# Kernel optimization log

Hardware: AMD Instinct MI355X
Metric: run time of the kernel (lower is better)

Reference implementation:

```python
import jax, jax.numpy as jnp
import numpy as np

COST_CLASS, COST_OBJECTNESS, COST_GIOU, COST_CENTER = 1.0, 0.5, 2.0, 1.0
B, Q, G, C = 32, 4096, 32, 128


def setup_inputs() -> dict:
    key = jax.random.key(0)
    ks = jax.random.split(key, 6)
    return {
        "sem_cls_prob": jax.random.uniform(ks[0], (B, Q, C), jnp.float32),
        "objectness_prob": jax.random.uniform(ks[1], (B, Q), jnp.float32),
        "center_dist": jax.random.uniform(ks[2], (B, Q, G), jnp.float32),
        "gious": jax.random.uniform(ks[3], (B, Q, G), jnp.float32) * 2.0 - 1.0,  # gIoU in [-1,1]
        "gt_box_sem_cls_label": jax.random.randint(ks[4], (B, G), 0, C).astype(jnp.int64),
        "nactual_gt": jax.random.randint(ks[5], (B,), 1, G + 1).astype(jnp.int64),
    }


def _lsa(Cmat):
    """Jonker-Volgenant shortest augmenting path Hungarian.
    Cmat: [n, m] float64 with n <= m. Returns p: [m+1] int64, p[j] = row matched
    to column j (or -1), index m is the virtual start column. Equivalent to
    scipy.optimize.linear_sum_assignment on Cmat (modulo ties)."""
    n, m = Cmat.shape
    u = np.zeros(n, np.float64)
    v = np.zeros(m + 1, np.float64)
    p = np.full(m + 1, -1, np.int64)
    way = np.zeros(m, np.int64)
    for i in range(n):
        p[m] = i
        j0 = m
        minv = np.full(m, np.inf)
        used = np.zeros(m + 1, bool)
        while True:
            used[j0] = True
            i0 = p[j0]
            cur = Cmat[i0] - u[i0] - v[:m]            # vectorized Dijkstra relaxation
            better = (~used[:m]) & (cur < minv)
            minv = np.where(better, cur, minv)
            way = np.where(better, j0, way)
            mv = np.where(used[:m], np.inf, minv)
            j1 = int(np.argmin(mv))
            delta = mv[j1]
            rows = p[used]                            # matched rows of used cols (distinct)
            u[rows] += delta
            v[used] -= delta
            minv = np.where(used[:m], minv, minv - delta)
            j0 = j1
            if p[j0] == -1:
                break
        while j0 != m:                                # augment along the path
            j1 = way[j0]
            p[j0] = p[j1]
            j0 = j1
    return p


def hungarian_assign(final_cost, nactual_gt):
    """final_cost: np [B,Q,G]; emulates the per-batch scipy loop of the module."""
    Bn, Qn, _ = final_cost.shape
    per_prop = np.zeros((Bn, Qn), np.int64)
    mask = np.zeros((Bn, Qn), np.float32)
    for b in range(Bn):
        ng = int(nactual_gt[b])
        if ng > 0:
            p = _lsa(final_cost[b, :, :ng].T.astype(np.float64))  # [ng, Q]
            cols = np.nonzero(p[:Qn] >= 0)[0]
            per_prop[b, cols] = p[cols]
            mask[b, cols] = 1.0
    return per_prop, mask


def build_cost(sem_cls_prob, objectness_prob, center_dist, gious, gt_box_sem_cls_label):
    Bn, Qn, _ = sem_cls_prob.shape
    Gn = gt_box_sem_cls_label.shape[1]
    idx = jnp.broadcast_to(gt_box_sem_cls_label[:, None, :], (Bn, Qn, Gn))
    class_mat = -jnp.take_along_axis(sem_cls_prob, idx, axis=2)        # [B,Q,G]
    return (COST_CLASS * class_mat
            - COST_OBJECTNESS * objectness_prob[:, :, None]
            + COST_CENTER * center_dist
            - COST_GIOU * gious)


def reference(sem_cls_prob, objectness_prob, center_dist, gious, gt_box_sem_cls_label, nactual_gt):
    final_cost = build_cost(sem_cls_prob, objectness_prob, center_dist, gious, gt_box_sem_cls_label)
    cost_np = np.asarray(jax.device_get(final_cost))
    per_prop, mask = hungarian_assign(cost_np, np.asarray(jax.device_get(nactual_gt)))
    return jnp.asarray(per_prop), jnp.asarray(mask)
```

## Files before the change

kernel.cpp:

```cpp
#include <hip/hip_runtime.h>
#include <math.h>

#define NB   32
#define BQ   4096
#define GMAX 32
#define NC   128
#define BS   512
#define CPT  (BQ / BS)
#define NWAVE (BS / 64)

#define TQ   32
#define BBS  256

__launch_bounds__(BBS)
__global__ void build_cost_kernel(const float* __restrict__ sem,
                                  const float* __restrict__ objp,
                                  const float* __restrict__ cent,
                                  const float* __restrict__ giou,
                                  const int*   __restrict__ labels,
                                  const int*   __restrict__ nact,
                                  float* __restrict__ cost)
{
    const int b  = blockIdx.y;
    const int q0 = blockIdx.x * TQ;
    const int tid = threadIdx.x;

    __shared__ float sem_sh[TQ][NC + 1];
    __shared__ float cent_sh[TQ][GMAX + 1];
    __shared__ float giou_sh[TQ][GMAX + 1];
    __shared__ int lab_sh[GMAX];

    if (tid < GMAX) lab_sh[tid] = labels[b * GMAX + tid];
    const int ng = nact[b];

    const float4* semb = (const float4*)(sem + ((size_t)b * BQ + q0) * NC);
#pragma unroll
    for (int r = tid; r < TQ * NC / 4; r += BBS) {
        float4 vv = semb[r];
        int e = r * 4;
        int qq = e >> 7;
        int cc = e & (NC - 1);
        sem_sh[qq][cc]     = vv.x;
        sem_sh[qq][cc + 1] = vv.y;
        sem_sh[qq][cc + 2] = vv.z;
        sem_sh[qq][cc + 3] = vv.w;
    }
    {
        const float4* centb = (const float4*)(cent + ((size_t)b * BQ + q0) * GMAX);
        const float4* gioub = (const float4*)(giou + ((size_t)b * BQ + q0) * GMAX);
        int r = tid;
        float4 cv = centb[r];
        float4 gv = gioub[r];
        int e = r * 4;
        int qq = e >> 5;
        int ii = e & (GMAX - 1);
        cent_sh[qq][ii]     = cv.x;
        cent_sh[qq][ii + 1] = cv.y;
        cent_sh[qq][ii + 2] = cv.z;
        cent_sh[qq][ii + 3] = cv.w;
        giou_sh[qq][ii]     = gv.x;
        giou_sh[qq][ii + 1] = gv.y;
        giou_sh[qq][ii + 2] = gv.z;
        giou_sh[qq][ii + 3] = gv.w;
    }
    __syncthreads();

    const int qi = tid & (TQ - 1);
    const int ig = tid >> 5;
    const int q  = q0 + qi;
    const float ho = __fmul_rn(0.5f, objp[b * BQ + q]);

    for (int i = ig; i < ng; i += 8) {
        float pcls = sem_sh[qi][lab_sh[i]];
        float ce   = cent_sh[qi][i];
        float gi   = giou_sh[qi][i];
        float c = __fsub_rn(__fadd_rn(__fsub_rn(-pcls, ho), ce),
                            __fmul_rn(2.0f, gi));
        cost[((size_t)b * GMAX + i) * BQ + q] = c;
    }
}

__launch_bounds__(BS, 1)
__global__ void matcher_kernel(const float* __restrict__ cost,
                               const int*   __restrict__ nact,
                               float* __restrict__ out)
{
    const int b    = blockIdx.x;
    const int tid  = threadIdx.x;
    const int m    = BQ;
    const int wave = tid >> 6;
    const int lane = tid & 63;

    __shared__ __align__(16) short p_lds[BQ + 8];
    __shared__ __align__(16) unsigned short way_lds[BQ];
    __shared__ double u_lds[GMAX];
    __shared__ double   redv[2][NWAVE];
    __shared__ unsigned redpk[2][NWAVE];
    __shared__ int    step_i0[GMAX + 2];
    __shared__ double step_D[GMAX + 2];
    __shared__ float  rmin_v[GMAX];
    __shared__ int    rmin_j[GMAX];
    __shared__ int    unmatched[GMAX];
    __shared__ int    s_nunm;

    for (int k = tid; k < BQ + 8; k += BS) p_lds[k] = -1;
    const int ng = nact[b];
    const float* cb = cost + (size_t)b * GMAX * BQ;
    __syncthreads();

    for (int r = wave; r < ng; r += NWAVE) {
        const float4* row4 = (const float4*)(cb + (size_t)r * BQ);
        float bv = INFINITY; int bj = 0;
#pragma unroll
        for (int it = 0; it < 16; it++) {
            float4 vv = row4[lane + 64 * it];
            int j = (lane + 64 * it) * 4;
            if (vv.x < bv) { bv = vv.x; bj = j; }
            if (vv.y < bv) { bv = vv.y; bj = j + 1; }
            if (vv.z < bv) { bv = vv.z; bj = j + 2; }
            if (vv.w < bv) { bv = vv.w; bj = j + 3; }
        }
#pragma unroll
        for (int off = 32; off >= 1; off >>= 1) {
            float ov = __shfl_down(bv, off, 64);
            int   oj = __shfl_down(bj, off, 64);
            if (ov < bv || (ov == bv && oj < bj)) { bv = ov; bj = oj; }
        }
        if (lane == 0) { rmin_v[r] = bv; rmin_j[r] = bj; }
    }
    __syncthreads();

    if (tid < ng) u_lds[tid] = (double)rmin_v[tid];
    if (tid == 0) {
        int nu = 0;
        for (int i = 0; i < ng; i++) {
            int j = rmin_j[i];
            if (p_lds[j] < 0) p_lds[j] = (short)i;
            else unmatched[nu++] = i;
        }
        s_nunm = nu;
    }
    __syncthreads();
    const int nunm = s_nunm;

    const double INF = (double)INFINITY;
    const int jbase = tid * CPT;
    const float4* cb4 = (const float4*)cb;

    double v_reg[CPT], minv[CPT], enterD[CPT];
    int way_reg[CPT], p_reg[CPT];
#pragma unroll
    for (int k = 0; k < CPT; k++) { v_reg[k] = 0.0; way_reg[k] = m; enterD[k] = 0.0; }

    for (int t = 0; t < nunm; t++) {
        const int ri = unmatched[t];

        int4 pv = ((const int4*)p_lds)[tid];
        p_reg[0] = (int)(short)(pv.x & 0xFFFF); p_reg[1] = pv.x >> 16;
        p_reg[2] = (int)(short)(pv.y & 0xFFFF); p_reg[3] = pv.y >> 16;
        p_reg[4] = (int)(short)(pv.z & 0xFFFF); p_reg[5] = pv.z >> 16;
        p_reg[6] = (int)(short)(pv.w & 0xFFFF); p_reg[7] = pv.w >> 16;

        const float4* r4 = cb4 + (size_t)ri * (BQ / 4) + tid * 2;
        float4 c0 = r4[0];
        float4 c1 = r4[1];
        double ui0 = u_lds[ri];

#pragma unroll
        for (int k = 0; k < CPT; k++) minv[k] = INF;
        unsigned used_mask = 0;
        int i0 = ri, j0 = m, ns = 0, buf = 0, jfin;
        double D = 0.0;

        while (true) {
            float cf[CPT] = {c0.x, c0.y, c0.z, c0.w, c1.x, c1.y, c1.z, c1.w};

            double bestv = INF;
            unsigned bestpk = ((unsigned)m << 8);
#pragma unroll
            for (int k = 0; k < CPT; k++) {
                bool un = !((used_mask >> k) & 1u);
                double cur = ((double)cf[k] - ui0) - v_reg[k];
                bool better = un && (cur < minv[k]);
                if (better) { minv[k] = cur; way_reg[k] = j0; }
                double mv = un ? minv[k] : INF;
                if (mv < bestv) {
                    bestv = mv;
                    bestpk = (((unsigned)(jbase + k)) << 8) | (unsigned)(p_reg[k] + 1);
                }
            }

#pragma unroll
            for (int off = 32; off >= 1; off >>= 1) {
                double   ov  = __shfl_down(bestv, off, 64);
                unsigned opk = __shfl_down(bestpk, off, 64);
                if (ov < bestv || (ov == bestv && opk < bestpk)) { bestv = ov; bestpk = opk; }
            }
            if (lane == 0) { redv[buf][wave] = bestv; redpk[buf][wave] = bestpk; }
            __syncthreads();

            double delta = redv[buf][0]; unsigned pk = redpk[buf][0];
#pragma unroll
            for (int w = 1; w < NWAVE; w++) {
                double ov = redv[buf][w]; unsigned opk = redpk[buf][w];
                if (ov < delta || (ov == delta && opk < pk)) { delta = ov; pk = opk; }
            }
            const int j1 = (int)(pk >> 8);
            const int pi = (int)(pk & 0xFFu) - 1;

            if (tid == 0) { step_i0[ns] = i0; step_D[ns] = D; }
            D += delta;
            ns++;

            if (pi < 0) { jfin = j1; break; }

            const float4* n4 = cb4 + (size_t)pi * (BQ / 4) + tid * 2;
            c0 = n4[0];
            c1 = n4[1];
            ui0 = u_lds[pi];

#pragma unroll
            for (int k = 0; k < CPT; k++)
                if (!((used_mask >> k) & 1u)) minv[k] -= delta;

            unsigned kk = (unsigned)(j1 - jbase);
            if (kk < CPT) { used_mask |= (1u << kk); enterD[kk] = D; }

            i0 = pi; j0 = j1; buf ^= 1;
        }

#pragma unroll
        for (int k = 0; k < CPT; k++)
            if ((used_mask >> k) & 1u) { v_reg[k] -= (D - enterD[k]); }
#pragma unroll
        for (int k = 0; k < CPT; k++) used_mask = 0;

        int4 wv;
        wv.x = (way_reg[0] & 0xFFFF) | (way_reg[1] << 16);
        wv.y = (way_reg[2] & 0xFFFF) | (way_reg[3] << 16);
        wv.z = (way_reg[4] & 0xFFFF) | (way_reg[5] << 16);
        wv.w = (way_reg[6] & 0xFFFF) | (way_reg[7] << 16);
        ((int4*)way_lds)[tid] = wv;

        __syncthreads();
        if (tid < ns) u_lds[step_i0[tid]] += D - step_D[tid];
        if (tid == 0) {
            int jc = jfin;
            while (jc != m) {
                int jp = (int)way_lds[jc];
                p_lds[jc] = (jp == m) ? (short)ri : p_lds[jp];
                jc = jp;
            }
        }
        __syncthreads();
    }

#pragma unroll
    for (int k = 0; k < CPT; k++) {
        int j = jbase + k;
        short pj = p_lds[j];
        out[(size_t)b * BQ + j] = (pj >= 0) ? (float)pj : 0.0f;
        out[(size_t)NB * BQ + (size_t)b * BQ + j] = (pj >= 0) ? 1.0f : 0.0f;
    }
}

extern "C" void kernel_launch(void* const* d_in, const int* in_sizes, int n_in,
                              void* d_out, int out_size, void* d_ws, size_t ws_size,
                              hipStream_t stream) {
    const float* sem    = (const float*)d_in[0];
    const float* objp   = (const float*)d_in[1];
    const float* cent   = (const float*)d_in[2];
    const float* giou   = (const float*)d_in[3];
    const int*   labels = (const int*)d_in[4];
    const int*   nact   = (const int*)d_in[5];
    float* out  = (float*)d_out;
    float* cost = (float*)d_ws;

    dim3 bgrid(BQ / TQ, NB);
    build_cost_kernel<<<bgrid, BBS, 0, stream>>>(sem, objp, cent, giou,
                                                 labels, nact, cost);
    matcher_kernel<<<NB, BS, 0, stream>>>(cost, nact, out);
}
```

Measured before the change: 142.2 us.

## Fuse row-min partials into cost build and software-pipeline tile loads

The cost-building kernel now handles eight query tiles per block, double-buffering shared memory and prefetching the next tile's inputs into registers while computing the current one. It also computes a per-tile row minimum with argmin for each GT row and writes it to a workspace array. The matcher then reduces 128 partials per row instead of rescanning the 4096-column cost row for its initial dual values. This trades a smaller grid and extra shuffles in the producer for less reading in the serial matcher prologue, and removes a redundant reset loop.

```diff
diff --git a/kernel.cpp b/kernel.cpp
--- a/kernel.cpp
+++ b/kernel.cpp
@@ -9,8 +9,10 @@
 #define CPT  (BQ / BS)
 #define NWAVE (BS / 64)
 
-#define TQ   32
-#define BBS  256
+#define TQ    32
+#define BBS   256
+#define TPB   8
+#define NTILE (BQ / TQ)
 
 __launch_bounds__(BBS)
 __global__ void build_cost_kernel(const float* __restrict__ sem,
@@ -19,70 +21,109 @@
                                   const float* __restrict__ giou,
                                   const int*   __restrict__ labels,
                                   const int*   __restrict__ nact,
-                                  float* __restrict__ cost)
+                                  float* __restrict__ cost,
+                                  float2* __restrict__ rowpart)
 {
-    const int b  = blockIdx.y;
-    const int q0 = blockIdx.x * TQ;
+    const int b   = blockIdx.y;
+    const int tg  = blockIdx.x;
     const int tid = threadIdx.x;
 
-    __shared__ float sem_sh[TQ][NC + 1];
-    __shared__ float cent_sh[TQ][GMAX + 1];
-    __shared__ float giou_sh[TQ][GMAX + 1];
+    __shared__ float sem_sh [2][TQ][NC + 1];
+    __shared__ float cent_sh[2][TQ][GMAX + 1];
+    __shared__ float giou_sh[2][TQ][GMAX + 1];
     __shared__ int lab_sh[GMAX];
 
     if (tid < GMAX) lab_sh[tid] = labels[b * GMAX + tid];
     const int ng = nact[b];
 
-    const float4* semb = (const float4*)(sem + ((size_t)b * BQ + q0) * NC);
-#pragma unroll
-    for (int r = tid; r < TQ * NC / 4; r += BBS) {
-        float4 vv = semb[r];
-        int e = r * 4;
-        int qq = e >> 7;
-        int cc = e & (NC - 1);
-        sem_sh[qq][cc]     = vv.x;
-        sem_sh[qq][cc + 1] = vv.y;
-        sem_sh[qq][cc + 2] = vv.z;
-        sem_sh[qq][cc + 3] = vv.w;
-    }
-    {
-        const float4* centb = (const float4*)(cent + ((size_t)b * BQ + q0) * GMAX);
-        const float4* gioub = (const float4*)(giou + ((size_t)b * BQ + q0) * GMAX);
-        int r = tid;
-        float4 cv = centb[r];
-        float4 gv = gioub[r];
-        int e = r * 4;
-        int qq = e >> 5;
-        int ii = e & (GMAX - 1);
-        cent_sh[qq][ii]     = cv.x;
-        cent_sh[qq][ii + 1] = cv.y;
-        cent_sh[qq][ii + 2] = cv.z;
-        cent_sh[qq][ii + 3] = cv.w;
-        giou_sh[qq][ii]     = gv.x;
-        giou_sh[qq][ii + 1] = gv.y;
-        giou_sh[qq][ii + 2] = gv.z;
-        giou_sh[qq][ii + 3] = gv.w;
-    }
-    __syncthreads();
-
     const int qi = tid & (TQ - 1);
     const int ig = tid >> 5;
-    const int q  = q0 + qi;
-    const float ho = __fmul_rn(0.5f, objp[b * BQ + q]);
-
-    for (int i = ig; i < ng; i += 8) {
-        float pcls = sem_sh[qi][lab_sh[i]];
-        float ce   = cent_sh[qi][i];
-        float gi   = giou_sh[qi][i];
-        float c = __fsub_rn(__fadd_rn(__fsub_rn(-pcls, ho), ce),
-                            __fmul_rn(2.0f, gi));
-        cost[((size_t)b * GMAX + i) * BQ + q] = c;
+
+    const size_t semoff = (size_t)b * BQ * NC;
+    const size_t cgoff  = (size_t)b * BQ * GMAX;
+    const int q0 = tg * (TPB * TQ);
+
+    float4 sr[4], cr, gr;
+    {
+        const float4* s4 = (const float4*)(sem + semoff + (size_t)q0 * NC);
+#pragma unroll
+        for (int x = 0; x < 4; x++) sr[x] = s4[x * BBS + tid];
+        const float4* c4 = (const float4*)(cent + cgoff + (size_t)q0 * GMAX);
+        const float4* g4 = (const float4*)(giou + cgoff + (size_t)q0 * GMAX);
+        cr = c4[tid];
+        gr = g4[tid];
+    }
+    float ho[TPB];
+#pragma unroll
+    for (int tt = 0; tt < TPB; tt++)
+        ho[tt] = __fmul_rn(0.5f, objp[b * BQ + q0 + tt * TQ + qi]);
+
+#pragma unroll
+    for (int tt = 0; tt < TPB; tt++) {
+        const int buf = tt & 1;
+        const int qt  = q0 + tt * TQ;
+
+#pragma unroll
+        for (int x = 0; x < 4; x++) {
+            int e  = (x * BBS + tid) * 4;
+            int qq = e >> 7, cc = e & (NC - 1);
+            sem_sh[buf][qq][cc]     = sr[x].x;
+            sem_sh[buf][qq][cc + 1] = sr[x].y;
+            sem_sh[buf][qq][cc + 2] = sr[x].z;
+            sem_sh[buf][qq][cc + 3] = sr[x].w;
+        }
+        {
+            int e = tid * 4, qq = e >> 5, ii = e & (GMAX - 1);
+            cent_sh[buf][qq][ii]     = cr.x;
+            cent_sh[buf][qq][ii + 1] = cr.y;
+            cent_sh[buf][qq][ii + 2] = cr.z;
+            cent_sh[buf][qq][ii + 3] = cr.w;
+            giou_sh[buf][qq][ii]     = gr.x;
+            giou_sh[buf][qq][ii + 1] = gr.y;
+            giou_sh[buf][qq][ii + 2] = gr.z;
+            giou_sh[buf][qq][ii + 3] = gr.w;
+        }
+        __syncthreads();
+
+        if (tt + 1 < TPB) {
+            const int qn = q0 + (tt + 1) * TQ;
+            const float4* s4 = (const float4*)(sem + semoff + (size_t)qn * NC);
+#pragma unroll
+            for (int x = 0; x < 4; x++) sr[x] = s4[x * BBS + tid];
+            const float4* c4 = (const float4*)(cent + cgoff + (size_t)qn * GMAX);
+            const float4* g4 = (const float4*)(giou + cgoff + (size_t)qn * GMAX);
+            cr = c4[tid];
+            gr = g4[tid];
+        }
+
+        const int q = qt + qi;
+        const float hob = ho[tt];
+        for (int i = ig; i < ng; i += 8) {
+            float pcls = sem_sh[buf][qi][lab_sh[i]];
+            float ce   = cent_sh[buf][qi][i];
+            float gi   = giou_sh[buf][qi][i];
+            float c = __fsub_rn(__fadd_rn(__fsub_rn(-pcls, hob), ce),
+                                __fmul_rn(2.0f, gi));
+            cost[((size_t)b * GMAX + i) * BQ + q] = c;
+
+            float bv = c; int bj = q;
+#pragma unroll
+            for (int off = 16; off >= 1; off >>= 1) {
+                float ov = __shfl_down(bv, off, 32);
+                int   oj = __shfl_down(bj, off, 32);
+                if (ov < bv || (ov == bv && oj < bj)) { bv = ov; bj = oj; }
+            }
+            if (qi == 0)
+                rowpart[((size_t)b * GMAX + i) * NTILE + (tg * TPB + tt)] =
+                    make_float2(bv, __int_as_float(bj));
+        }
     }
 }
 
 __launch_bounds__(BS, 1)
-__global__ void matcher_kernel(const float* __restrict__ cost,
-                               const int*   __restrict__ nact,
+__global__ void matcher_kernel(const float*  __restrict__ cost,
+                               const float2* __restrict__ rowpart,
+                               const int*    __restrict__ nact,
                                float* __restrict__ out)
 {
     const int b    = blockIdx.x;
@@ -109,17 +150,12 @@
     __syncthreads();
 
     for (int r = wave; r < ng; r += NWAVE) {
-        const float4* row4 = (const float4*)(cb + (size_t)r * BQ);
-        float bv = INFINITY; int bj = 0;
-#pragma unroll
-        for (int it = 0; it < 16; it++) {
-            float4 vv = row4[lane + 64 * it];
-            int j = (lane + 64 * it) * 4;
-            if (vv.x < bv) { bv = vv.x; bj = j; }
-            if (vv.y < bv) { bv = vv.y; bj = j + 1; }
-            if (vv.z < bv) { bv = vv.z; bj = j + 2; }
-            if (vv.w < bv) { bv = vv.w; bj = j + 3; }
-        }
+        const float4* rp4 =
+            (const float4*)(rowpart + ((size_t)b * GMAX + r) * NTILE);
+        float4 pp = rp4[lane];
+        float bv = pp.x; int bj = __float_as_int(pp.y);
+        float v2 = pp.z; int j2 = __float_as_int(pp.w);
+        if (v2 < bv || (v2 == bv && j2 < bj)) { bv = v2; bj = j2; }
 #pragma unroll
         for (int off = 32; off >= 1; off >>= 1) {
             float ov = __shfl_down(bv, off, 64);
@@ -231,9 +267,7 @@
 
 #pragma unroll
         for (int k = 0; k < CPT; k++)
-            if ((used_mask >> k) & 1u) { v_reg[k] -= (D - enterD[k]); }
-#pragma unroll
-        for (int k = 0; k < CPT; k++) used_mask = 0;
+            if ((used_mask >> k) & 1u) v_reg[k] -= (D - enterD[k]);
 
         int4 wv;
         wv.x = (way_reg[0] & 0xFFFF) | (way_reg[1] << 16);
@@ -274,10 +308,11 @@
     const int*   labels = (const int*)d_in[4];
     const int*   nact   = (const int*)d_in[5];
     float* out  = (float*)d_out;
-    float* cost = (float*)d_ws;
-
-    dim3 bgrid(BQ / TQ, NB);
+    float*  cost    = (float*)d_ws;
+    float2* rowpart = (float2*)((char*)d_ws + (size_t)16 * 1024 * 1024);
+
+    dim3 bgrid(NTILE / TPB, NB);
     build_cost_kernel<<<bgrid, BBS, 0, stream>>>(sem, objp, cent, giou,
-                                                 labels, nact, cost);
-    matcher_kernel<<<NB, BS, 0, stream>>>(cost, nact, out);
+                                                 labels, nact, cost, rowpart);
+    matcher_kernel<<<NB, BS, 0, stream>>>(cost, rowpart, nact, out);
 }
```

After: 146.2 us. 2.8% more time.
